# Optimization experiments

Hardware: AMD Instinct MI355X
Metric: run time of the kernel (lower is better)

Reference implementation:

```python
import jax, jax.numpy as jnp
import numpy as np

B, N, C, H = 4, 4096, 128, 4


def setup_inputs() -> dict:
    key = jax.random.key(0)
    ks = jax.random.split(key, 12)
    def rn(k, shape, s=0.02):
        return jax.random.normal(k, shape, jnp.float32) * s
    return dict(
        x=jax.random.normal(ks[0], (B, N, C), jnp.float32),
        p=jax.random.normal(ks[1], (B, N, 3), jnp.float32),
        fcl1_w=rn(ks[2], (C, C)), fcl1_b=jnp.zeros((C,), jnp.float32),
        # per-head (stacked over leading H axis) TransformerLayer params
        hq_w=rn(ks[3], (H, C, C)), hq_b=jnp.zeros((H, C), jnp.float32),
        hk_w=rn(ks[4], (H, C, C)), hk_b=jnp.zeros((H, C), jnp.float32),
        hv_w=rn(ks[5], (H, C, C)), hv_b=jnp.zeros((H, C), jnp.float32),
        pe1_w=rn(ks[6], (H, C, 3)), pe1_b=jnp.zeros((H, C), jnp.float32),  # Conv1d(3->C, k=1)
        pe2_w=rn(ks[7], (H, C, C)), pe2_b=jnp.zeros((H, C), jnp.float32),  # Conv1d(C->C, k=1)
        mh_w=rn(ks[8], (C, 4 * C)), mh_b=jnp.zeros((C,), jnp.float32),
        fcl2_w=rn(ks[9], (C, C)), fcl2_b=jnp.zeros((C,), jnp.float32),
    )


def reference(x, p, fcl1_w, fcl1_b, hq_w, hq_b, hk_w, hk_b, hv_w, hv_b,
              pe1_w, pe1_b, pe2_w, pe2_b, mh_w, mh_b, fcl2_w, fcl2_b):
    residual = x
    xf = x @ fcl1_w.T + fcl1_b  # fcl1
    scale = 1.0 / jnp.sqrt(jnp.asarray(C, jnp.float32))

    def head(qw, qb, kw, kb, vw, vb, p1w, p1b, p2w, p2b):
        # kernel-size-1 Conv1d == pointwise linear over coords
        pe = jax.nn.relu(jnp.einsum('bnd,cd->bnc', p, p1w) + p1b)
        pe = jnp.einsum('bnc,dc->bnd', pe, p2w) + p2b
        xh = xf + pe
        q = xh @ kw.T + kb  # note: original uses self.key for x_query
        k = xh @ qw.T + qb  # and self.query for x_key (name swap, kept faithful)
        v = xh @ vw.T + vb
        s = jax.nn.softmax(jnp.einsum('bnc,bmc->bnm', q, k) * scale, axis=-1)
        return jnp.einsum('bnm,bmc->bnc', s, v)

    outs = jax.vmap(head)(hq_w, hq_b, hk_w, hk_b, hv_w, hv_b,
                          pe1_w, pe1_b, pe2_w, pe2_b)  # [H,B,N,C]
    cat = jnp.moveaxis(outs, 0, 2).reshape(B, N, H * C)  # concat head1..head4 on last dim
    y = cat @ mh_w.T + mh_b
    y = y @ fcl2_w.T + fcl2_b
    mu = jnp.mean(y, axis=-1, keepdims=True)
    var = jnp.var(y, axis=-1, keepdims=True)
    y = (y - mu) / jnp.sqrt(var + 1e-5)  # torch.layer_norm, no affine
    return (y + residual, p)
```

## Files before the change

kernel.cpp:

```cpp
#include <hip/hip_runtime.h>
#include <hip/hip_bf16.h>

typedef __bf16 bf16;
typedef bf16 bf16x8 __attribute__((ext_vector_type(8)));
typedef float f32x4 __attribute__((ext_vector_type(4)));

static __device__ __forceinline__ f32x4 mfma16(bf16x8 a, bf16x8 b, f32x4 c) {
  return __builtin_amdgcn_mfma_f32_16x16x32_bf16(a, b, c, 0, 0, 0);
}

typedef __attribute__((address_space(3))) void lds_t;
typedef const __attribute__((address_space(1))) void gm_t;

#define N_SEG 18
#define TOTAL_CONV 2511616

__global__ void probe_k(const unsigned short* __restrict__ xr, int* __restrict__ flag) {
  int wild = 0;
#pragma unroll
  for (int i = 0; i < 8; i++) {
    unsigned short w = xr[threadIdx.x * 8 + i];
    int e = (w >> 7) & 0xFF;
    if (e < 110 || e > 134) wild++;
  }
#pragma unroll
  for (int off = 1; off < 64; off <<= 1) wild += __shfl_xor(wild, off);
  if (threadIdx.x == 0) *flag = (wild > 64) ? 1 : 0;
}

struct ConvArgs { const void* src[N_SEG]; };

__global__ __launch_bounds__(256) void convall_k(ConvArgs a, bf16* __restrict__ dst,
                                                 void* __restrict__ outp,
                                                 const int* __restrict__ flag) {
  const int ends[N_SEG] = {2097152, 2146304, 2162688, 2162816, 2228352, 2228864,
                           2294400, 2294912, 2360448, 2360960, 2362496, 2363008,
                           2428544, 2429056, 2494592, 2495104, 2511488, 2511616};
  int i = blockIdx.x * 256 + threadIdx.x;
  if (i >= TOTAL_CONV) {
    int j = i - TOTAL_CONV;
    if (j < 49152) {
      if (*flag) ((float*)outp)[2097152 + j] = ((const float*)a.src[1])[j];
      else       ((bf16*)outp)[2097152 + j]  = ((const bf16*)a.src[1])[j];
    }
    return;
  }
  int s = 0;
  while (i >= ends[s]) s++;
  int j = i - (s ? ends[s - 1] : 0);
  if (*flag) dst[i] = (bf16)((const float*)a.src[s])[j];
  else       dst[i] = ((const bf16*)a.src[s])[j];
}

__global__ __launch_bounds__(256, 2) void pre_k(
    const bf16* __restrict__ x, const bf16* __restrict__ p,
    const bf16* __restrict__ f1w, const bf16* __restrict__ f1b,
    const bf16* __restrict__ pe1w, const bf16* __restrict__ pe1b,
    const bf16* __restrict__ pe2w, const bf16* __restrict__ pe2b,
    const bf16* __restrict__ Wq, const bf16* __restrict__ Bq,
    const bf16* __restrict__ Wk, const bf16* __restrict__ Bk,
    const bf16* __restrict__ Wv, const bf16* __restrict__ Bv,
    bf16* __restrict__ qo, bf16* __restrict__ ko, bf16* __restrict__ vo)
{
  const int lane = threadIdx.x & 63;
  const int wave = threadIdx.x >> 6;
  const int quad = lane >> 4;
  const int n15 = lane & 15;
  const int h = blockIdx.y;
  const int r0 = blockIdx.x * 64;
  const int wr = wave * 16;

  __shared__ bf16 tile[9216];

  f32x4 acc[8];
  const f32x4 zz = {};

  {
    bf16x8 ap = {};
    if (quad == 0) {
      const bf16* pr = p + (long)(r0 + wr + n15) * 3;
      ap[0] = pr[0]; ap[1] = pr[1]; ap[2] = pr[2];
    }
#pragma unroll
    for (int ct = 0; ct < 8; ct++) {
      bf16x8 bw = {};
      if (quad == 0) {
        const bf16* wp = pe1w + ((long)h * 128 + ct * 16 + n15) * 3;
        bw[0] = wp[0]; bw[1] = wp[1]; bw[2] = wp[2];
      }
      acc[ct] = mfma16(ap, bw, zz);
    }
#pragma unroll
    for (int ct = 0; ct < 8; ct++) {
      const int col = ct * 16 + n15;
      const float bb = (float)pe1b[h * 128 + col];
#pragma unroll
      for (int r = 0; r < 4; r++)
        tile[(wr + quad * 4 + r) * 136 + col] = (bf16)fmaxf(acc[ct][r] + bb, 0.f);
    }
  }

#pragma unroll
  for (int ct = 0; ct < 8; ct++) acc[ct] = zz;
#pragma unroll
  for (int kk = 0; kk < 4; kk++) {
    const int ka = kk * 32 + quad * 8;
    bf16x8 a0 = *(const bf16x8*)&tile[(wr + n15) * 136 + ka];
#pragma unroll
    for (int ct = 0; ct < 8; ct++) {
      bf16x8 wf = *(const bf16x8*)(pe2w + (long)h * 16384 + (long)(ct * 16 + n15) * 128 + ka);
      acc[ct] = mfma16(a0, wf, acc[ct]);
    }
  }
#pragma unroll
  for (int kk = 0; kk < 4; kk++) {
    const int ka = kk * 32 + quad * 8;
    bf16x8 a0 = *(const bf16x8*)(x + (long)(r0 + wr + n15) * 128 + ka);
#pragma unroll
    for (int ct = 0; ct < 8; ct++) {
      bf16x8 wf = *(const bf16x8*)(f1w + (long)(ct * 16 + n15) * 128 + ka);
      acc[ct] = mfma16(a0, wf, acc[ct]);
    }
  }
#pragma unroll
  for (int ct = 0; ct < 8; ct++) {
    const int col = ct * 16 + n15;
    const float bv = (float)pe2b[h * 128 + col] + (float)f1b[col];
#pragma unroll
    for (int r = 0; r < 4; r++)
      tile[(wr + quad * 4 + r) * 136 + col] = (bf16)(acc[ct][r] + bv);
  }

  bf16x8 af[4];
#pragma unroll
  for (int kk = 0; kk < 4; kk++)
    af[kk] = *(const bf16x8*)&tile[(wr + n15) * 136 + kk * 32 + quad * 8];

#pragma unroll
  for (int m = 0; m < 2; m++) {
    f32x4 a2[8];
#pragma unroll
    for (int ct = 0; ct < 8; ct++) a2[ct] = zz;
    const bf16* Wm = (m == 0) ? Wq : Wk;
#pragma unroll
    for (int kk = 0; kk < 4; kk++) {
      const int ka = kk * 32 + quad * 8;
#pragma unroll
      for (int ct = 0; ct < 8; ct++) {
        bf16x8 wf = *(const bf16x8*)(Wm + (long)h * 16384 + (long)(ct * 16 + n15) * 128 + ka);
        a2[ct] = mfma16(af[kk], wf, a2[ct]);
      }
    }
    bf16* oz = ((m == 0) ? qo : ko) + (long)h * 2097152;
    const bf16* Bz = (m == 0) ? Bq : Bk;
    const float sc = (m == 0) ? 0.08838834764831845f : 1.0f;
#pragma unroll
    for (int ct = 0; ct < 8; ct++) {
      const int col = ct * 16 + n15;
      const float bv = (float)Bz[h * 128 + col];
#pragma unroll
      for (int r = 0; r < 4; r++)
        oz[(long)(r0 + wr + quad * 4 + r) * 128 + col] = (bf16)((a2[ct][r] + bv) * sc);
    }
  }

  {
    f32x4 a2[8];
#pragma unroll
    for (int ct = 0; ct < 8; ct++) a2[ct] = zz;
#pragma unroll
    for (int kk = 0; kk < 4; kk++) {
      const int ka = kk * 32 + quad * 8;
#pragma unroll
      for (int ct = 0; ct < 8; ct++) {
        bf16x8 wf = *(const bf16x8*)(Wv + (long)h * 16384 + (long)(ct * 16 + n15) * 128 + ka);
        a2[ct] = mfma16(af[kk], wf, a2[ct]);
      }
    }
    __syncthreads();
#pragma unroll
    for (int ct = 0; ct < 8; ct++) {
      const int col = ct * 16 + n15;
      const float bv = (float)Bv[h * 128 + col];
#pragma unroll
      for (int r = 0; r < 4; r++)
        tile[col * 72 + (wr + quad * 4 + r)] = (bf16)(a2[ct][r] + bv);
    }
    __syncthreads();
    bf16* vz = vo + (long)h * 2097152;
#pragma unroll
    for (int i = 0; i < 16; i++) {
      const int c = wave * 32 + i * 2 + (lane >> 5);
      const int m2 = (lane & 31) * 2;
      *(unsigned int*)&vz[(long)c * 16384 + r0 + m2] =
          *(const unsigned int*)&tile[c * 72 + m2];
    }
  }
}

__global__ __launch_bounds__(256, 2) void attn_k(
    const bf16* __restrict__ Q, const bf16* __restrict__ Kg,
    const bf16* __restrict__ vT, bf16* __restrict__ Op, float* __restrict__ ls)
{
  const int lane = threadIdx.x & 63;
  const int wave = threadIdx.x >> 6;
  const int quad = lane >> 4;
  const int n15 = lane & 15;
  const int qt = blockIdx.x >> 1;
  const int half = blockIdx.x & 1;
  const int b = blockIdx.y, h = blockIdx.z;
  const long qkBase = ((long)h * 4 + b) * 4096 * 128;
  const long vBase = (long)h * (128L * 16384) + (long)b * 4096;
  const int wrow = qt * 128 + wave * 32;
  const int kvStart = half * 2048;

  __shared__ bf16 Kt[64 * 128];
  __shared__ bf16 Vt[128 * 64];
  __shared__ bf16 Pt[8][1024];

  const bf16* qrow = Q + qkBase + (long)(wrow + n15) * 128 + quad * 8;

  const int krl  = lane >> 4;
  const int kpch = lane & 15;
  const int vcl  = lane >> 3;
  const int vpch = lane & 7;

  f32x4 Om[2][8] = {};
  float l_part[2][4] = {};

  for (int kv0 = kvStart; kv0 < kvStart + 2048; kv0 += 64) {
    __syncthreads();
#pragma unroll
    for (int i = 0; i < 4; i++) {
      const int row = wave * 16 + i * 4 + krl;
      const int ch = kpch ^ (row & 15);
      __builtin_amdgcn_global_load_lds(
          (gm_t*)(Kg + qkBase + (long)(kv0 + row) * 128 + ch * 8),
          (lds_t*)&Kt[(wave * 16 + i * 4) * 128], 16, 0, 0);
    }
#pragma unroll
    for (int i = 0; i < 4; i++) {
      const int c = wave * 32 + i * 8 + vcl;
      const int vch = vpch ^ (c & 7);
      __builtin_amdgcn_global_load_lds(
          (gm_t*)(vT + vBase + (long)c * 16384 + kv0 + vch * 8),
          (lds_t*)&Vt[(wave * 32 + i * 8) * 64], 16, 0, 0);
    }
    __syncthreads();

    f32x4 S[2][4] = {};
#pragma unroll
    for (int kk = 0; kk < 4; kk++) {
      bf16x8 q0 = *(const bf16x8*)(qrow + kk * 32);
      bf16x8 q1 = *(const bf16x8*)(qrow + 2048 + kk * 32);
#pragma unroll
      for (int ct = 0; ct < 4; ct++) {
        bf16x8 kf = *(const bf16x8*)&Kt[(ct * 16 + n15) * 128 + (((kk * 4 + quad) ^ n15) * 8)];
        S[0][ct] = mfma16(q0, kf, S[0][ct]);
        S[1][ct] = mfma16(q1, kf, S[1][ct]);
      }
    }

#pragma unroll
    for (int g = 0; g < 2; g++)
#pragma unroll
      for (int ct = 0; ct < 4; ct++)
#pragma unroll
        for (int r = 0; r < 4; r++) {
          float e = __expf(S[g][ct][r]);
          l_part[g][r] += e;
          const int row = quad * 4 + r;
          const int kv = ct * 16 + n15;
          Pt[wave * 2 + g][row * 64 + ((((kv >> 3) ^ (row & 7)) * 8)) + (kv & 7)] = (bf16)e;
        }

#pragma unroll
    for (int kk = 0; kk < 2; kk++) {
      bf16x8 vf[8];
#pragma unroll
      for (int ct = 0; ct < 8; ct++) {
        const int c = ct * 16 + n15;
        vf[ct] = *(const bf16x8*)&Vt[c * 64 + (((kk * 4 + quad) ^ (c & 7)) * 8)];
      }
#pragma unroll
      for (int g = 0; g < 2; g++) {
        bf16x8 pf = *(const bf16x8*)&Pt[wave * 2 + g][n15 * 64 + (((kk * 4 + quad) ^ (n15 & 7)) * 8)];
#pragma unroll
        for (int ct = 0; ct < 8; ct++)
          Om[g][ct] = mfma16(pf, vf[ct], Om[g][ct]);
      }
    }
  }

#pragma unroll
  for (int g = 0; g < 2; g++) {
#pragma unroll
    for (int r = 0; r < 4; r++) {
      float s = l_part[g][r];
#pragma unroll
      for (int off = 1; off < 16; off <<= 1) s += __shfl_xor(s, off);
      if (n15 == 0)
        ls[((long)half * 4 + h) * 16384 + b * 4096 + wrow + g * 16 + quad * 4 + r] = s;
    }
    const long ob = (long)half * 8388608 + (long)(b * 4096 + wrow + g * 16 + quad * 4) * 512 + h * 128;
#pragma unroll
    for (int ct = 0; ct < 8; ct++)
#pragma unroll
      for (int r = 0; r < 4; r++)
        Op[ob + (long)r * 512 + ct * 16 + n15] = (bf16)Om[g][ct][r];
  }
}

__global__ __launch_bounds__(256) void tail_k(
    const bf16* __restrict__ Op, const float* __restrict__ ls,
    const bf16* __restrict__ mhw, const bf16* __restrict__ mhb,
    const bf16* __restrict__ f2w, const bf16* __restrict__ f2b,
    const void* __restrict__ xraw, void* __restrict__ outraw,
    const int* __restrict__ flag)
{
  const int lane = threadIdx.x & 63;
  const int wave = threadIdx.x >> 6;
  const int quad = lane >> 4;
  const int n15 = lane & 15;
  const int r0 = blockIdx.x * 64 + wave * 16;
  __shared__ bf16 y1t[64][136];

  float invA[4];
#pragma unroll
  for (int hh = 0; hh < 4; hh++) {
    const float l0 = ls[(long)hh * 16384 + r0 + n15];
    const float l1 = ls[(long)(4 + hh) * 16384 + r0 + n15];
    invA[hh] = 1.f / (l0 + l1);
  }

  f32x4 acc[8] = {};
  for (int k0 = 0; k0 < 512; k0 += 32) {
    const int hh = k0 >> 7;
    const int ka = k0 + quad * 8;
    bf16x8 v0 = *(const bf16x8*)(Op + (long)(r0 + n15) * 512 + ka);
    bf16x8 v1 = *(const bf16x8*)(Op + 8388608L + (long)(r0 + n15) * 512 + ka);
    bf16x8 a0;
#pragma unroll
    for (int j = 0; j < 8; j++)
      a0[j] = (bf16)(((float)v0[j] + (float)v1[j]) * invA[hh]);
#pragma unroll
    for (int ct = 0; ct < 8; ct++) {
      bf16x8 wf = *(const bf16x8*)(mhw + (long)(ct * 16 + n15) * 512 + ka);
      acc[ct] = mfma16(a0, wf, acc[ct]);
    }
  }
#pragma unroll
  for (int ct = 0; ct < 8; ct++) {
    const float bv = (float)mhb[ct * 16 + n15];
#pragma unroll
    for (int r = 0; r < 4; r++)
      y1t[wave * 16 + quad * 4 + r][ct * 16 + n15] = (bf16)(acc[ct][r] + bv);
  }

  f32x4 acc2[8] = {};
  for (int k0 = 0; k0 < 128; k0 += 32) {
    const int ka = k0 + quad * 8;
    bf16x8 a0 = *(const bf16x8*)&y1t[wave * 16 + n15][ka];
#pragma unroll
    for (int ct = 0; ct < 8; ct++) {
      bf16x8 wf = *(const bf16x8*)(f2w + (long)(ct * 16 + n15) * 128 + ka);
      acc2[ct] = mfma16(a0, wf, acc2[ct]);
    }
  }

  float s1[4] = {}, s2[4] = {};
#pragma unroll
  for (int ct = 0; ct < 8; ct++) {
    const float bv = (float)f2b[ct * 16 + n15];
#pragma unroll
    for (int r = 0; r < 4; r++) {
      const float v = acc2[ct][r] + bv;
      acc2[ct][r] = v;
      s1[r] += v;
      s2[r] += v * v;
    }
  }
  float mu[4], inv[4];
#pragma unroll
  for (int r = 0; r < 4; r++) {
    float a = s1[r], b2 = s2[r];
#pragma unroll
    for (int off = 1; off < 16; off <<= 1) {
      a += __shfl_xor(a, off);
      b2 += __shfl_xor(b2, off);
    }
    mu[r] = a * (1.f / 128.f);
    const float var = fmaxf(b2 * (1.f / 128.f) - mu[r] * mu[r], 0.f);
    inv[r] = rsqrtf(var + 1e-5f);
  }

  const int isF32 = *flag;
#pragma unroll
  for (int ct = 0; ct < 8; ct++)
#pragma unroll
    for (int r = 0; r < 4; r++) {
      const long idx = (long)(r0 + quad * 4 + r) * 128 + ct * 16 + n15;
      const float resid = isF32 ? ((const float*)xraw)[idx]
                                : (float)((const bf16*)xraw)[idx];
      const float v = (acc2[ct][r] - mu[r]) * inv[r] + resid;
      if (isF32) ((float*)outraw)[idx] = v;
      else       ((bf16*)outraw)[idx] = (bf16)v;
    }
}

extern "C" void kernel_launch(void* const* d_in, const int* in_sizes, int n_in,
                              void* d_out, int out_size, void* d_ws, size_t ws_size,
                              hipStream_t stream)
{
  bf16* ws  = (bf16*)d_ws;
  bf16* q   = ws;
  bf16* kb  = ws + 8388608;
  bf16* vt  = ws + 16777216;
  bf16* Op  = ws + 25165824;
  float* lsb = (float*)(ws + 41943040);
  const long AR = 42205184;
  int* flag = (int*)(ws + 44720000);

  static const int counts[N_SEG] = {2097152, 49152, 16384, 128, 65536, 512, 65536, 512,
                                    65536, 512, 1536, 512, 65536, 512, 65536, 512, 16384, 128};
  long offs[N_SEG]; long o = AR;
  for (int i = 0; i < N_SEG; i++) { offs[i] = o; o += counts[i]; }
  bf16* xc    = ws + offs[0];
  bf16* pc    = ws + offs[1];
  bf16* f1w   = ws + offs[2];
  bf16* f1b   = ws + offs[3];
  bf16* hqw   = ws + offs[4];
  bf16* hqb   = ws + offs[5];
  bf16* hkw   = ws + offs[6];
  bf16* hkb   = ws + offs[7];
  bf16* hvw   = ws + offs[8];
  bf16* hvb   = ws + offs[9];
  bf16* pe1w  = ws + offs[10];
  bf16* pe1b  = ws + offs[11];
  bf16* pe2w  = ws + offs[12];
  bf16* pe2b  = ws + offs[13];
  bf16* mhw   = ws + offs[14];
  bf16* mhb   = ws + offs[15];
  bf16* f2w   = ws + offs[16];
  bf16* f2b   = ws + offs[17];

  probe_k<<<dim3(1), dim3(64), 0, stream>>>((const unsigned short*)d_in[0], flag);
  ConvArgs ca;
  for (int i = 0; i < N_SEG; i++) ca.src[i] = d_in[i];
  convall_k<<<dim3((TOTAL_CONV + 49152 + 255) / 256), dim3(256), 0, stream>>>(ca, ws + AR, d_out, flag);

  dim3 blk(256);
  pre_k<<<dim3(256, 4), blk, 0, stream>>>(xc, pc, f1w, f1b, pe1w, pe1b, pe2w, pe2b,
                                          hkw, hkb, hqw, hqb, hvw, hvb, q, kb, vt);
  attn_k<<<dim3(64, 4, 4), blk, 0, stream>>>(q, kb, vt, Op, lsb);
  tail_k<<<dim3(256), blk, 0, stream>>>(Op, lsb, mhw, mhb, f2w, f2b, d_in[0], d_out, flag);
}
```

Before: 366.8 us.

## Drop KV split in attention, normalize in-kernel, fold dtype probe into convert

The attention kernel no longer splits the KV range in two halves with partial outputs and row sums written to workspace. Each wave now handles 16 query rows over the full KV range with Q held in registers, uses exp2 with log2e folded into the Q scale, and writes normalized output directly. The tail kernel skips the two-partial merge, and the separate dtype probe kernel is merged into the conversion kernel. This cuts workspace traffic and one launch, but each block now does twice the KV work with half the rows, which lowers reuse of each K/V tile per block.

```diff
diff --git a/kernel.cpp b/kernel.cpp
--- a/kernel.cpp
+++ b/kernel.cpp
@@ -15,32 +15,35 @@
 #define N_SEG 18
 #define TOTAL_CONV 2511616
 
-__global__ void probe_k(const unsigned short* __restrict__ xr, int* __restrict__ flag) {
-  int wild = 0;
-#pragma unroll
-  for (int i = 0; i < 8; i++) {
-    unsigned short w = xr[threadIdx.x * 8 + i];
-    int e = (w >> 7) & 0xFF;
-    if (e < 110 || e > 134) wild++;
-  }
-#pragma unroll
-  for (int off = 1; off < 64; off <<= 1) wild += __shfl_xor(wild, off);
-  if (threadIdx.x == 0) *flag = (wild > 64) ? 1 : 0;
-}
-
 struct ConvArgs { const void* src[N_SEG]; };
 
 __global__ __launch_bounds__(256) void convall_k(ConvArgs a, bf16* __restrict__ dst,
                                                  void* __restrict__ outp,
-                                                 const int* __restrict__ flag) {
+                                                 int* __restrict__ flag) {
   const int ends[N_SEG] = {2097152, 2146304, 2162688, 2162816, 2228352, 2228864,
                            2294400, 2294912, 2360448, 2360960, 2362496, 2363008,
                            2428544, 2429056, 2494592, 2495104, 2511488, 2511616};
+  const unsigned short* xr = (const unsigned short*)a.src[0];
+  int wild = 0;
+#pragma unroll
+  for (int j = 0; j < 2; j++) {
+    unsigned short w = xr[threadIdx.x * 2 + j];
+    int e = (w >> 7) & 0xFF;
+    if (e < 110 || e > 134) wild++;
+  }
+#pragma unroll
+  for (int off = 1; off < 64; off <<= 1) wild += __shfl_xor(wild, off);
+  __shared__ int red[4];
+  if ((threadIdx.x & 63) == 0) red[threadIdx.x >> 6] = wild;
+  __syncthreads();
+  const int isF32 = (red[0] + red[1] + red[2] + red[3]) > 64;
+  if (blockIdx.x == 0 && threadIdx.x == 0) *flag = isF32;
+
   int i = blockIdx.x * 256 + threadIdx.x;
   if (i >= TOTAL_CONV) {
     int j = i - TOTAL_CONV;
     if (j < 49152) {
-      if (*flag) ((float*)outp)[2097152 + j] = ((const float*)a.src[1])[j];
+      if (isF32) ((float*)outp)[2097152 + j] = ((const float*)a.src[1])[j];
       else       ((bf16*)outp)[2097152 + j]  = ((const bf16*)a.src[1])[j];
     }
     return;
@@ -48,7 +51,7 @@
   int s = 0;
   while (i >= ends[s]) s++;
   int j = i - (s ? ends[s - 1] : 0);
-  if (*flag) dst[i] = (bf16)((const float*)a.src[s])[j];
+  if (isF32) dst[i] = (bf16)((const float*)a.src[s])[j];
   else       dst[i] = ((const bf16*)a.src[s])[j];
 }
 
@@ -153,7 +156,7 @@
     }
     bf16* oz = ((m == 0) ? qo : ko) + (long)h * 2097152;
     const bf16* Bz = (m == 0) ? Bq : Bk;
-    const float sc = (m == 0) ? 0.08838834764831845f : 1.0f;
+    const float sc = (m == 0) ? 0.12751743f : 1.0f;
 #pragma unroll
     for (int ct = 0; ct < 8; ct++) {
       const int col = ct * 16 + n15;
@@ -200,35 +203,35 @@
 
 __global__ __launch_bounds__(256, 2) void attn_k(
     const bf16* __restrict__ Q, const bf16* __restrict__ Kg,
-    const bf16* __restrict__ vT, bf16* __restrict__ Op, float* __restrict__ ls)
+    const bf16* __restrict__ vT, bf16* __restrict__ cat)
 {
   const int lane = threadIdx.x & 63;
   const int wave = threadIdx.x >> 6;
   const int quad = lane >> 4;
   const int n15 = lane & 15;
-  const int qt = blockIdx.x >> 1;
-  const int half = blockIdx.x & 1;
   const int b = blockIdx.y, h = blockIdx.z;
   const long qkBase = ((long)h * 4 + b) * 4096 * 128;
   const long vBase = (long)h * (128L * 16384) + (long)b * 4096;
-  const int wrow = qt * 128 + wave * 32;
-  const int kvStart = half * 2048;
+  const int wrow = blockIdx.x * 64 + wave * 16;
 
   __shared__ bf16 Kt[64 * 128];
   __shared__ bf16 Vt[128 * 64];
-  __shared__ bf16 Pt[8][1024];
-
-  const bf16* qrow = Q + qkBase + (long)(wrow + n15) * 128 + quad * 8;
+  __shared__ bf16 Pt[4][1024];
+
+  bf16x8 qf[4];
+#pragma unroll
+  for (int kk = 0; kk < 4; kk++)
+    qf[kk] = *(const bf16x8*)(Q + qkBase + (long)(wrow + n15) * 128 + kk * 32 + quad * 8);
 
   const int krl  = lane >> 4;
   const int kpch = lane & 15;
   const int vcl  = lane >> 3;
   const int vpch = lane & 7;
 
-  f32x4 Om[2][8] = {};
-  float l_part[2][4] = {};
-
-  for (int kv0 = kvStart; kv0 < kvStart + 2048; kv0 += 64) {
+  f32x4 Om[8] = {};
+  float l_part[4] = {};
+
+  for (int kv0 = 0; kv0 < 4096; kv0 += 64) {
     __syncthreads();
 #pragma unroll
     for (int i = 0; i < 4; i++) {
@@ -248,71 +251,57 @@
     }
     __syncthreads();
 
-    f32x4 S[2][4] = {};
+    f32x4 S[4] = {};
 #pragma unroll
     for (int kk = 0; kk < 4; kk++) {
-      bf16x8 q0 = *(const bf16x8*)(qrow + kk * 32);
-      bf16x8 q1 = *(const bf16x8*)(qrow + 2048 + kk * 32);
 #pragma unroll
       for (int ct = 0; ct < 4; ct++) {
         bf16x8 kf = *(const bf16x8*)&Kt[(ct * 16 + n15) * 128 + (((kk * 4 + quad) ^ n15) * 8)];
-        S[0][ct] = mfma16(q0, kf, S[0][ct]);
-        S[1][ct] = mfma16(q1, kf, S[1][ct]);
-      }
-    }
-
-#pragma unroll
-    for (int g = 0; g < 2; g++)
-#pragma unroll
-      for (int ct = 0; ct < 4; ct++)
-#pragma unroll
-        for (int r = 0; r < 4; r++) {
-          float e = __expf(S[g][ct][r]);
-          l_part[g][r] += e;
-          const int row = quad * 4 + r;
-          const int kv = ct * 16 + n15;
-          Pt[wave * 2 + g][row * 64 + ((((kv >> 3) ^ (row & 7)) * 8)) + (kv & 7)] = (bf16)e;
-        }
+        S[ct] = mfma16(qf[kk], kf, S[ct]);
+      }
+    }
+
+#pragma unroll
+    for (int ct = 0; ct < 4; ct++)
+#pragma unroll
+      for (int r = 0; r < 4; r++) {
+        float e = __builtin_amdgcn_exp2f(S[ct][r]);
+        l_part[r] += e;
+        const int row = quad * 4 + r;
+        const int kv = ct * 16 + n15;
+        Pt[wave][row * 64 + ((((kv >> 3) ^ (row & 7)) * 8)) + (kv & 7)] = (bf16)e;
+      }
 
 #pragma unroll
     for (int kk = 0; kk < 2; kk++) {
-      bf16x8 vf[8];
+      bf16x8 pf = *(const bf16x8*)&Pt[wave][n15 * 64 + (((kk * 4 + quad) ^ (n15 & 7)) * 8)];
 #pragma unroll
       for (int ct = 0; ct < 8; ct++) {
         const int c = ct * 16 + n15;
-        vf[ct] = *(const bf16x8*)&Vt[c * 64 + (((kk * 4 + quad) ^ (c & 7)) * 8)];
-      }
-#pragma unroll
-      for (int g = 0; g < 2; g++) {
-        bf16x8 pf = *(const bf16x8*)&Pt[wave * 2 + g][n15 * 64 + (((kk * 4 + quad) ^ (n15 & 7)) * 8)];
-#pragma unroll
-        for (int ct = 0; ct < 8; ct++)
-          Om[g][ct] = mfma16(pf, vf[ct], Om[g][ct]);
-      }
-    }
-  }
-
-#pragma unroll
-  for (int g = 0; g < 2; g++) {
-#pragma unroll
-    for (int r = 0; r < 4; r++) {
-      float s = l_part[g][r];
-#pragma unroll
-      for (int off = 1; off < 16; off <<= 1) s += __shfl_xor(s, off);
-      if (n15 == 0)
-        ls[((long)half * 4 + h) * 16384 + b * 4096 + wrow + g * 16 + quad * 4 + r] = s;
-    }
-    const long ob = (long)half * 8388608 + (long)(b * 4096 + wrow + g * 16 + quad * 4) * 512 + h * 128;
-#pragma unroll
-    for (int ct = 0; ct < 8; ct++)
-#pragma unroll
-      for (int r = 0; r < 4; r++)
-        Op[ob + (long)r * 512 + ct * 16 + n15] = (bf16)Om[g][ct][r];
-  }
+        bf16x8 vf = *(const bf16x8*)&Vt[c * 64 + (((kk * 4 + quad) ^ (c & 7)) * 8)];
+        Om[ct] = mfma16(pf, vf, Om[ct]);
+      }
+    }
+  }
+
+  float inv[4];
+#pragma unroll
+  for (int r = 0; r < 4; r++) {
+    float s = l_part[r];
+#pragma unroll
+    for (int off = 1; off < 16; off <<= 1) s += __shfl_xor(s, off);
+    inv[r] = 1.f / s;
+  }
+  const long ob = ((long)b * 4096 + wrow + quad * 4) * 512 + h * 128;
+#pragma unroll
+  for (int ct = 0; ct < 8; ct++)
+#pragma unroll
+    for (int r = 0; r < 4; r++)
+      cat[ob + (long)r * 512 + ct * 16 + n15] = (bf16)(Om[ct][r] * inv[r]);
 }
 
 __global__ __launch_bounds__(256) void tail_k(
-    const bf16* __restrict__ Op, const float* __restrict__ ls,
+    const bf16* __restrict__ cat,
     const bf16* __restrict__ mhw, const bf16* __restrict__ mhb,
     const bf16* __restrict__ f2w, const bf16* __restrict__ f2b,
     const void* __restrict__ xraw, void* __restrict__ outraw,
@@ -325,24 +314,10 @@
   const int r0 = blockIdx.x * 64 + wave * 16;
   __shared__ bf16 y1t[64][136];
 
-  float invA[4];
-#pragma unroll
-  for (int hh = 0; hh < 4; hh++) {
-    const float l0 = ls[(long)hh * 16384 + r0 + n15];
-    const float l1 = ls[(long)(4 + hh) * 16384 + r0 + n15];
-    invA[hh] = 1.f / (l0 + l1);
-  }
-
   f32x4 acc[8] = {};
   for (int k0 = 0; k0 < 512; k0 += 32) {
-    const int hh = k0 >> 7;
     const int ka = k0 + quad * 8;
-    bf16x8 v0 = *(const bf16x8*)(Op + (long)(r0 + n15) * 512 + ka);
-    bf16x8 v1 = *(const bf16x8*)(Op + 8388608L + (long)(r0 + n15) * 512 + ka);
-    bf16x8 a0;
-#pragma unroll
-    for (int j = 0; j < 8; j++)
-      a0[j] = (bf16)(((float)v0[j] + (float)v1[j]) * invA[hh]);
+    bf16x8 a0 = *(const bf16x8*)(cat + (long)(r0 + n15) * 512 + ka);
 #pragma unroll
     for (int ct = 0; ct < 8; ct++) {
       bf16x8 wf = *(const bf16x8*)(mhw + (long)(ct * 16 + n15) * 512 + ka);
@@ -416,10 +391,9 @@
   bf16* q   = ws;
   bf16* kb  = ws + 8388608;
   bf16* vt  = ws + 16777216;
-  bf16* Op  = ws + 25165824;
-  float* lsb = (float*)(ws + 41943040);
-  const long AR = 42205184;
-  int* flag = (int*)(ws + 44720000);
+  bf16* cat = ws + 25165824;
+  const long AR = 33554432;
+  int* flag = (int*)(ws + 36066048);
 
   static const int counts[N_SEG] = {2097152, 49152, 16384, 128, 65536, 512, 65536, 512,
                                     65536, 512, 1536, 512, 65536, 512, 65536, 512, 16384, 128};
@@ -444,7 +418,6 @@
   bf16* f2w   = ws + offs[16];
   bf16* f2b   = ws + offs[17];
 
-  probe_k<<<dim3(1), dim3(64), 0, stream>>>((const unsigned short*)d_in[0], flag);
   ConvArgs ca;
   for (int i = 0; i < N_SEG; i++) ca.src[i] = d_in[i];
   convall_k<<<dim3((TOTAL_CONV + 49152 + 255) / 256), dim3(256), 0, stream>>>(ca, ws + AR, d_out, flag);
@@ -452,6 +425,6 @@
   dim3 blk(256);
   pre_k<<<dim3(256, 4), blk, 0, stream>>>(xc, pc, f1w, f1b, pe1w, pe1b, pe2w, pe2b,
                                           hkw, hkb, hqw, hqb, hvw, hvb, q, kb, vt);
-  attn_k<<<dim3(64, 4, 4), blk, 0, stream>>>(q, kb, vt, Op, lsb);
-  tail_k<<<dim3(256), blk, 0, stream>>>(Op, lsb, mhw, mhb, f2w, f2b, d_in[0], d_out, flag);
-}
+  attn_k<<<dim3(64, 4, 4), blk, 0, stream>>>(q, kb, vt, cat);
+  tail_k<<<dim3(256), blk, 0, stream>>>(cat, mhw, mhb, f2w, f2b, d_in[0], d_out, flag);
+}
```

New measurement: 379.9 us. 3.6% more time.
